# Kernel tuning notes

Hardware: AMD Instinct MI355X
Metric: run time of the kernel (lower is better)

The kernel has to match this reference:

```python
import jax, jax.numpy as jnp
import numpy as np

B, T, F, H = 16, 512, 32, 128
EPS = 1e-5


def _layer_norm(y, g, b):
    mu = jnp.mean(y, axis=-1, keepdims=True)
    var = jnp.mean(jnp.square(y - mu), axis=-1, keepdims=True)
    return (y - mu) * jax.lax.rsqrt(var + EPS) * g + b


def setup_inputs() -> dict:
    key = jax.random.key(0)
    ks = jax.random.split(key, 16)
    s = 0.1  # small param scale
    return {
        "x": jax.random.normal(ks[0], (B, T, F), jnp.float32),
        # weight GRN (input_size == hidden == F, skip is Identity)
        "wg_fc1_w": jax.random.normal(ks[1], (F, F), jnp.float32) * s,
        "wg_fc1_b": jnp.zeros((F,), jnp.float32),
        "wg_fc2_w": jax.random.normal(ks[2], (2 * F, F), jnp.float32) * s,
        "wg_fc2_b": jnp.zeros((2 * F,), jnp.float32),
        "wg_ln_g": jnp.ones((F,), jnp.float32),
        "wg_ln_b": jnp.zeros((F,), jnp.float32),
        # per-feature GRNs (input_size=1 -> hidden H), batched over F
        "f_fc1_w": jax.random.normal(ks[3], (F, H), jnp.float32) * s,   # torch Linear(1,H).weight squeezed
        "f_fc1_b": jax.random.normal(ks[4], (F, H), jnp.float32) * s,
        "f_fc2_w": jax.random.normal(ks[5], (F, 2 * H, H), jnp.float32) * s,
        "f_fc2_b": jax.random.normal(ks[6], (F, 2 * H), jnp.float32) * s,
        "f_skip_w": jax.random.normal(ks[7], (F, H), jnp.float32) * s,  # Linear(1,H).weight squeezed
        "f_skip_b": jax.random.normal(ks[8], (F, H), jnp.float32) * s,
        "f_ln_g": jnp.ones((F, H), jnp.float32),
        "f_ln_b": jnp.zeros((F, H), jnp.float32),
    }


def reference(x, wg_fc1_w, wg_fc1_b, wg_fc2_w, wg_fc2_b, wg_ln_g, wg_ln_b,
              f_fc1_w, f_fc1_b, f_fc2_w, f_fc2_b, f_skip_w, f_skip_b,
              f_ln_g, f_ln_b):
    # --- weight GRN over the feature axis: [B,T,F] -> [B,T,F] ---
    h = jax.nn.elu(jnp.einsum('btf,gf->btg', x, wg_fc1_w) + wg_fc1_b)
    h2 = jnp.einsum('btg,kg->btk', h, wg_fc2_w) + wg_fc2_b  # [B,T,2F]
    a, g = jnp.split(h2, 2, axis=-1)
    glu = a * jax.nn.sigmoid(g)
    weights = jax.nn.softmax(_layer_norm(x + glu, wg_ln_g, wg_ln_b), axis=-1)  # [B,T,F]

    # --- all F per-feature GRNs batched (input width 1) ---
    xe = x[..., None]                                   # [B,T,F,1]
    h = jax.nn.elu(xe * f_fc1_w + f_fc1_b)              # [B,T,F,H]
    h2 = jnp.einsum('btfh,fgh->btfg', h, f_fc2_w) + f_fc2_b  # [B,T,F,2H]
    a, g = jnp.split(h2, 2, axis=-1)
    glu = a * jax.nn.sigmoid(g)                         # [B,T,F,H]
    res = xe * f_skip_w + f_skip_b                      # [B,T,F,H]
    y = _layer_norm(res + glu, f_ln_g, f_ln_b)          # per-feature LN params [F,H]

    # --- softmax-weighted combine ---
    return jnp.einsum('btf,btfh->bth', weights, y)      # [B,T,H]
```

## Files before the change

kernel.cpp:

```cpp
#include <hip/hip_runtime.h>
#include <cstdint>
#include <cstddef>

#define EPS 1e-5f

typedef float    f4    __attribute__((ext_vector_type(4)));
typedef _Float16 half8 __attribute__((ext_vector_type(8)));
typedef _Float16 half4 __attribute__((ext_vector_type(4)));

#define S_XS 33
#define LOG2E 1.44269504088896f

#define GLD_LDS16(gp, lp)                                        \
    __builtin_amdgcn_global_load_lds(                            \
        (const __attribute__((address_space(1))) void*)(gp),     \
        (__attribute__((address_space(3))) void*)(lp), 16, 0, 0)

__device__ __forceinline__ float fexp(float x)  { return __builtin_amdgcn_exp2f(x * LOG2E); }
__device__ __forceinline__ float frcp(float x)  { return __builtin_amdgcn_rcpf(x); }
__device__ __forceinline__ float frsq(float x)  { return __builtin_amdgcn_rsqf(x); }
__device__ __forceinline__ float fsig(float g)  { return frcp(1.f + __builtin_amdgcn_exp2f(g * -LOG2E)); }
__device__ __forceinline__ float felu(float t)  { return t > 0.f ? t : fexp(t) - 1.f; }

__global__ __launch_bounds__(256) void k_prep(
    const float* __restrict__ in_w2, _Float16* __restrict__ w2c,
    const float* __restrict__ x, const float* __restrict__ w1,
    const float* __restrict__ b1, const float* __restrict__ w2,
    const float* __restrict__ b2, const float* __restrict__ lng,
    const float* __restrict__ lnb,
    float* __restrict__ x_t, float* __restrict__ wts_t)
{
    __shared__ float w1s[32 * S_XS];
    __shared__ float w2s[64 * S_XS];
    __shared__ float xsW[32 * S_XS];
    __shared__ float ytile[32 * S_XS];

    const int bid = blockIdx.x;
    const int tid = threadIdx.x;

    if (bid < 512) {
        int t = bid * 256 + tid;
        int q  = t & 3;
        int g  = (t >> 2) & 255;
        int fk = t >> 10;
        int f = fk >> 2, kq = fk & 3;
        const float* ip = in_w2 + ((size_t)f * 256 + g) * 128 + kq * 32 + q * 8;
        f4 v0 = *(const f4*)ip, v1 = *(const f4*)(ip + 4);
        half8 h;
        #pragma unroll
        for (int i = 0; i < 4; ++i) { h[i] = (_Float16)v0[i]; h[4 + i] = (_Float16)v1[i]; }
        *(half8*)(w2c + (size_t)fk * 8192 + q * 2048 + g * 8) = h;
        return;
    }

    const int lane = tid & 63;
    const int f = lane & 31;
    const int wv = tid >> 6;
    const int row0 = (bid - 512) * 32;

    for (int i = tid; i < 1024; i += 256) {
        int r = i >> 5, c = i & 31;
        w1s[r * S_XS + c] = w1[i];
        xsW[r * S_XS + c] = x[(size_t)row0 * 32 + i];
    }
    for (int i = tid; i < 2048; i += 256) {
        int r = i >> 5, c = i & 31;
        w2s[r * S_XS + c] = w2[i];
    }
    const float b1f = b1[f], b2a = b2[f], b2g = b2[f + 32];
    const float lgf = lng[f], lbf = lnb[f];
    __syncthreads();

    for (int rr = 0; rr < 8; ++rr) {
        const int r = wv * 8 + rr;
        float acc = b1f;
        #pragma unroll
        for (int k = 0; k < 32; ++k)
            acc = fmaf(w1s[f * S_XS + k], xsW[r * S_XS + k], acc);
        float hval = felu(acc);

        float a = b2a, g = b2g;
        #pragma unroll
        for (int k = 0; k < 32; ++k) {
            float hk = __shfl(hval, k, 64);
            a = fmaf(w2s[f * S_XS + k], hk, a);
            g = fmaf(w2s[(f + 32) * S_XS + k], hk, g);
        }
        float xv = xsW[r * S_XS + f];
        float v = xv + a * fsig(g);

        float s = v;
        #pragma unroll
        for (int o = 1; o < 64; o <<= 1) s += __shfl_xor(s, o, 64);
        float mu = s * (1.f / 64.f);
        float d = v - mu;
        float sq = d * d;
        #pragma unroll
        for (int o = 1; o < 64; o <<= 1) sq += __shfl_xor(sq, o, 64);
        float y = d * frsq(sq * (1.f / 64.f) + EPS) * lgf + lbf;

        float m = y;
        #pragma unroll
        for (int o = 1; o < 64; o <<= 1) m = fmaxf(m, __shfl_xor(m, o, 64));
        float e = fexp(y - m);
        float se = e;
        #pragma unroll
        for (int o = 1; o < 64; o <<= 1) se += __shfl_xor(se, o, 64);
        if (lane < 32) ytile[r * S_XS + f] = e * 2.f * frcp(se);
    }
    __syncthreads();
    for (int i = tid; i < 1024; i += 256) {
        int ff = i >> 5, r = i & 31;
        x_t[(size_t)ff * 8192 + row0 + r]   = xsW[r * S_XS + ff];
        wts_t[(size_t)ff * 8192 + row0 + r] = ytile[r * S_XS + ff];
    }
}

__global__ __launch_bounds__(256, 3) void k_main(
    const _Float16* __restrict__ w2c,
    const float* __restrict__ x_t,
    const float* __restrict__ wts_t,
    const float* __restrict__ fc1w, const float* __restrict__ fc1b,
    const float* __restrict__ fc2b,
    const float* __restrict__ skw, const float* __restrict__ skb,
    const float* __restrict__ lng, const float* __restrict__ lnb,
    float* __restrict__ out)
{
    __shared__ __align__(16) _Float16 bchunk[2][8192];

    const int tid = threadIdx.x;
    const int fbase = (blockIdx.x >> 7) * 4;
    const int row0 = (blockIdx.x & 127) * 64;

    const int lane = tid & 63;
    const int wv = tid >> 6;
    const int l15 = lane & 15;
    const int q = lane >> 4;
    const int boff = q * 2048 + l15 * 8;

    auto stage = [&](int c) {
        const _Float16* gp = w2c + ((size_t)(fbase + (c >> 2)) * 4 + (c & 3)) * 8192;
        #pragma unroll
        for (int r = 0; r < 4; ++r)
            GLD_LDS16(gp + (r * 256 + tid) * 8,
                      &bchunk[c & 1][(r * 256 + tid) * 8]);
    };

    float out_acc[8][4];
    #pragma unroll
    for (int nt = 0; nt < 8; ++nt)
        #pragma unroll
        for (int rg = 0; rg < 4; ++rg) out_acc[nt][rg] = 0.f;

    stage(0);
    __syncthreads();

    int c = 0;
    for (int fi = 0; fi < 4; ++fi) {
        const int f = fbase + fi;
        const float* xcol = x_t + (size_t)f * 8192 + row0 + wv * 16;
        const float* wcol = wts_t + (size_t)f * 8192 + row0 + wv * 16;
        const float xvA = xcol[l15];

        half8 A[4];
        #pragma unroll
        for (int kq = 0; kq < 4; ++kq) {
            const float* wp = fc1w + f * 128 + kq * 32 + 8 * q;
            const float* bp = fc1b + f * 128 + kq * 32 + 8 * q;
            f4 w0 = *(const f4*)wp, w1v = *(const f4*)(wp + 4);
            f4 b0 = *(const f4*)bp, b1v = *(const f4*)(bp + 4);
            #pragma unroll
            for (int j = 0; j < 4; ++j) {
                A[kq][j]     = (_Float16)felu(fmaf(xvA, w0[j], b0[j]));
                A[kq][4 + j] = (_Float16)felu(fmaf(xvA, w1v[j], b1v[j]));
            }
        }

        f4 acc[16];
        #pragma unroll
        for (int nt = 0; nt < 8; ++nt) {
            const int h = nt * 16 + l15;
            float ba = fc2b[f * 256 + h];
            float bg = fc2b[f * 256 + 128 + h];
            #pragma unroll
            for (int rg = 0; rg < 4; ++rg) { acc[nt][rg] = ba; acc[nt + 8][rg] = bg; }
        }

        #pragma unroll
        for (int kq = 0; kq < 4; ++kq, ++c) {
            if (c + 1 < 16) stage(c + 1);
            const _Float16* bb = &bchunk[c & 1][boff];
            #pragma unroll
            for (int nt = 0; nt < 16; ++nt) {
                half8 B = *(const half8*)(bb + nt * 128);
                acc[nt] = __builtin_amdgcn_mfma_f32_16x16x32_f16(A[kq], B, acc[nt], 0, 0, 0);
            }
            __syncthreads();
        }

        f4 xr = *(const f4*)(xcol + 4 * q);
        f4 wr = *(const f4*)(wcol + 4 * q);
        float s[4] = {0.f, 0.f, 0.f, 0.f}, sq[4] = {0.f, 0.f, 0.f, 0.f};
        #pragma unroll
        for (int nt = 0; nt < 8; ++nt) {
            const int h = nt * 16 + l15;
            float sw = skw[f * 128 + h];
            float sb = skb[f * 128 + h];
            #pragma unroll
            for (int rg = 0; rg < 4; ++rg) {
                float a = acc[nt][rg];
                float g = acc[nt + 8][rg];
                float val = fmaf(xr[rg], sw, sb) + a * fsig(g);
                acc[nt][rg] = val;
                s[rg] += val;
                sq[rg] = fmaf(val, val, sq[rg]);
            }
        }
        #pragma unroll
        for (int o = 1; o < 16; o <<= 1) {
            #pragma unroll
            for (int rg = 0; rg < 4; ++rg) {
                s[rg] += __shfl_xor(s[rg], o, 64);
                sq[rg] += __shfl_xor(sq[rg], o, 64);
            }
        }
        float mu[4], c1[4];
        #pragma unroll
        for (int rg = 0; rg < 4; ++rg) {
            mu[rg] = s[rg] * (1.f / 128.f);
            float var = sq[rg] * (1.f / 128.f) - mu[rg] * mu[rg];
            c1[rg] = wr[rg] * frsq(fmaxf(var, 0.f) + EPS);
        }
        #pragma unroll
        for (int nt = 0; nt < 8; ++nt) {
            const int h = nt * 16 + l15;
            float lg = lng[f * 128 + h];
            float lb = lnb[f * 128 + h];
            #pragma unroll
            for (int rg = 0; rg < 4; ++rg) {
                float u = (acc[nt][rg] - mu[rg]) * c1[rg];
                out_acc[nt][rg] = fmaf(u, lg, fmaf(wr[rg], lb, out_acc[nt][rg]));
            }
        }
    }

    #pragma unroll
    for (int nt = 0; nt < 8; ++nt) {
        #pragma unroll
        for (int rg = 0; rg < 4; ++rg) {
            const int r = row0 + wv * 16 + 4 * q + rg;
            atomicAdd(&out[(size_t)r * 128 + nt * 16 + l15], out_acc[nt][rg]);
        }
    }
}

extern "C" void kernel_launch(void* const* d_in, const int* in_sizes, int n_in,
                              void* d_out, int out_size, void* d_ws, size_t ws_size,
                              hipStream_t stream) {
    const float* x     = (const float*)d_in[0];
    const float* wg1w  = (const float*)d_in[1];
    const float* wg1b  = (const float*)d_in[2];
    const float* wg2w  = (const float*)d_in[3];
    const float* wg2b  = (const float*)d_in[4];
    const float* wglng = (const float*)d_in[5];
    const float* wglnb = (const float*)d_in[6];
    const float* fc1w  = (const float*)d_in[7];
    const float* fc1b  = (const float*)d_in[8];
    const float* fc2w  = (const float*)d_in[9];
    const float* fc2b  = (const float*)d_in[10];
    const float* skw   = (const float*)d_in[11];
    const float* skb   = (const float*)d_in[12];
    const float* lng   = (const float*)d_in[13];
    const float* lnb   = (const float*)d_in[14];
    float* out = (float*)d_out;

    char* ws = (char*)d_ws;
    _Float16* w2c = (_Float16*)ws;
    float* x_t    = (float*)(ws + (2u << 20));
    float* wts_t  = (float*)(ws + (3u << 20));

    k_prep<<<dim3(768), dim3(256), 0, stream>>>(fc2w, w2c, x, wg1w, wg1b,
                                                wg2w, wg2b, wglng, wglnb,
                                                x_t, wts_t);
    hipMemsetAsync(out, 0, (size_t)out_size * sizeof(float), stream);
    k_main<<<dim3(1024), dim3(256), 0, stream>>>(w2c, x_t, wts_t, fc1w, fc1b,
                                                 fc2b, skw, skb, lng, lnb, out);
}
```

Baseline: 164.8 us.

## Double rows per k_main block and fold output zeroing into prep kernel

Each k_main wave now processes two 16-row M-tiles that share every staged fc2 weight chunk, halving the grid to 512 blocks. Each block therefore stages half as much weight data from global memory per row, and LDS B-fragment reads are amortized over two MFMAs. Launch bounds drop to 2 blocks per CU to allow the doubled accumulator registers. The separate hipMemsetAsync is replaced by 16 extra zeroing blocks in k_prep, removing one stream operation. The risks are lower occupancy and fewer blocks to fill the GPU.

```diff
diff --git a/kernel.cpp b/kernel.cpp
--- a/kernel.cpp
+++ b/kernel.cpp
@@ -28,7 +28,8 @@
     const float* __restrict__ b1, const float* __restrict__ w2,
     const float* __restrict__ b2, const float* __restrict__ lng,
     const float* __restrict__ lnb,
-    float* __restrict__ x_t, float* __restrict__ wts_t)
+    float* __restrict__ x_t, float* __restrict__ wts_t,
+    float* __restrict__ outp)
 {
     __shared__ float w1s[32 * S_XS];
     __shared__ float w2s[64 * S_XS];
@@ -53,6 +54,14 @@
         return;
     }
 
+    if (bid >= 768) {
+        int t = (bid - 768) * 256 + tid;
+        f4 z; z[0] = 0.f; z[1] = 0.f; z[2] = 0.f; z[3] = 0.f;
+        for (int i = t; i < 262144; i += 4096)
+            *(f4*)(outp + (size_t)i * 4) = z;
+        return;
+    }
+
     const int lane = tid & 63;
     const int f = lane & 31;
     const int wv = tid >> 6;
@@ -116,7 +125,7 @@
     }
 }
 
-__global__ __launch_bounds__(256, 3) void k_main(
+__global__ __launch_bounds__(256, 2) void k_main(
     const _Float16* __restrict__ w2c,
     const float* __restrict__ x_t,
     const float* __restrict__ wts_t,
@@ -129,8 +138,8 @@
     __shared__ __align__(16) _Float16 bchunk[2][8192];
 
     const int tid = threadIdx.x;
-    const int fbase = (blockIdx.x >> 7) * 4;
-    const int row0 = (blockIdx.x & 127) * 64;
+    const int fbase = (blockIdx.x >> 6) * 4;
+    const int row0 = (blockIdx.x & 63) * 128;
 
     const int lane = tid & 63;
     const int wv = tid >> 6;
@@ -146,11 +155,13 @@
                       &bchunk[c & 1][(r * 256 + tid) * 8]);
     };
 
-    float out_acc[8][4];
+    float out_acc[2][8][4];
     #pragma unroll
-    for (int nt = 0; nt < 8; ++nt)
-        #pragma unroll
-        for (int rg = 0; rg < 4; ++rg) out_acc[nt][rg] = 0.f;
+    for (int ss = 0; ss < 2; ++ss)
+        #pragma unroll
+        for (int nt = 0; nt < 8; ++nt)
+            #pragma unroll
+            for (int rg = 0; rg < 4; ++rg) out_acc[ss][nt][rg] = 0.f;
 
     stage(0);
     __syncthreads();
@@ -158,11 +169,12 @@
     int c = 0;
     for (int fi = 0; fi < 4; ++fi) {
         const int f = fbase + fi;
-        const float* xcol = x_t + (size_t)f * 8192 + row0 + wv * 16;
-        const float* wcol = wts_t + (size_t)f * 8192 + row0 + wv * 16;
-        const float xvA = xcol[l15];
-
-        half8 A[4];
+        const float* xcol = x_t + (size_t)f * 8192 + row0 + wv * 32;
+        const float* wcol = wts_t + (size_t)f * 8192 + row0 + wv * 32;
+        const float xvA0 = xcol[l15];
+        const float xvA1 = xcol[16 + l15];
+
+        half8 A0[4], A1[4];
         #pragma unroll
         for (int kq = 0; kq < 4; ++kq) {
             const float* wp = fc1w + f * 128 + kq * 32 + 8 * q;
@@ -171,19 +183,28 @@
             f4 b0 = *(const f4*)bp, b1v = *(const f4*)(bp + 4);
             #pragma unroll
             for (int j = 0; j < 4; ++j) {
-                A[kq][j]     = (_Float16)felu(fmaf(xvA, w0[j], b0[j]));
-                A[kq][4 + j] = (_Float16)felu(fmaf(xvA, w1v[j], b1v[j]));
-            }
-        }
-
-        f4 acc[16];
+                float t0 = fmaf(xvA0, w0[j], b0[j]);
+                float t1 = fmaf(xvA0, w1v[j], b1v[j]);
+                A0[kq][j]     = (_Float16)felu(t0);
+                A0[kq][4 + j] = (_Float16)felu(t1);
+                float u0 = fmaf(xvA1, w0[j], b0[j]);
+                float u1 = fmaf(xvA1, w1v[j], b1v[j]);
+                A1[kq][j]     = (_Float16)felu(u0);
+                A1[kq][4 + j] = (_Float16)felu(u1);
+            }
+        }
+
+        f4 acc[2][16];
         #pragma unroll
         for (int nt = 0; nt < 8; ++nt) {
             const int h = nt * 16 + l15;
             float ba = fc2b[f * 256 + h];
             float bg = fc2b[f * 256 + 128 + h];
             #pragma unroll
-            for (int rg = 0; rg < 4; ++rg) { acc[nt][rg] = ba; acc[nt + 8][rg] = bg; }
+            for (int rg = 0; rg < 4; ++rg) {
+                acc[0][nt][rg] = ba; acc[0][nt + 8][rg] = bg;
+                acc[1][nt][rg] = ba; acc[1][nt + 8][rg] = bg;
+            }
         }
 
         #pragma unroll
@@ -193,63 +214,81 @@
             #pragma unroll
             for (int nt = 0; nt < 16; ++nt) {
                 half8 B = *(const half8*)(bb + nt * 128);
-                acc[nt] = __builtin_amdgcn_mfma_f32_16x16x32_f16(A[kq], B, acc[nt], 0, 0, 0);
+                acc[0][nt] = __builtin_amdgcn_mfma_f32_16x16x32_f16(A0[kq], B, acc[0][nt], 0, 0, 0);
+                acc[1][nt] = __builtin_amdgcn_mfma_f32_16x16x32_f16(A1[kq], B, acc[1][nt], 0, 0, 0);
             }
             __syncthreads();
         }
 
-        f4 xr = *(const f4*)(xcol + 4 * q);
-        f4 wr = *(const f4*)(wcol + 4 * q);
-        float s[4] = {0.f, 0.f, 0.f, 0.f}, sq[4] = {0.f, 0.f, 0.f, 0.f};
+        f4 xr[2], wr[2];
+        xr[0] = *(const f4*)(xcol + 4 * q);
+        xr[1] = *(const f4*)(xcol + 16 + 4 * q);
+        wr[0] = *(const f4*)(wcol + 4 * q);
+        wr[1] = *(const f4*)(wcol + 16 + 4 * q);
+        float s[2][4] = {{0.f,0.f,0.f,0.f},{0.f,0.f,0.f,0.f}};
+        float sq[2][4] = {{0.f,0.f,0.f,0.f},{0.f,0.f,0.f,0.f}};
         #pragma unroll
         for (int nt = 0; nt < 8; ++nt) {
             const int h = nt * 16 + l15;
             float sw = skw[f * 128 + h];
             float sb = skb[f * 128 + h];
             #pragma unroll
+            for (int ss = 0; ss < 2; ++ss) {
+                #pragma unroll
+                for (int rg = 0; rg < 4; ++rg) {
+                    float a = acc[ss][nt][rg];
+                    float g = acc[ss][nt + 8][rg];
+                    float val = fmaf(xr[ss][rg], sw, sb) + a * fsig(g);
+                    acc[ss][nt][rg] = val;
+                    s[ss][rg] += val;
+                    sq[ss][rg] = fmaf(val, val, sq[ss][rg]);
+                }
+            }
+        }
+        #pragma unroll
+        for (int o = 1; o < 16; o <<= 1) {
+            #pragma unroll
+            for (int ss = 0; ss < 2; ++ss)
+                #pragma unroll
+                for (int rg = 0; rg < 4; ++rg) {
+                    s[ss][rg] += __shfl_xor(s[ss][rg], o, 64);
+                    sq[ss][rg] += __shfl_xor(sq[ss][rg], o, 64);
+                }
+        }
+        float mu[2][4], c1[2][4];
+        #pragma unroll
+        for (int ss = 0; ss < 2; ++ss)
+            #pragma unroll
             for (int rg = 0; rg < 4; ++rg) {
-                float a = acc[nt][rg];
-                float g = acc[nt + 8][rg];
-                float val = fmaf(xr[rg], sw, sb) + a * fsig(g);
-                acc[nt][rg] = val;
-                s[rg] += val;
-                sq[rg] = fmaf(val, val, sq[rg]);
-            }
-        }
-        #pragma unroll
-        for (int o = 1; o < 16; o <<= 1) {
-            #pragma unroll
-            for (int rg = 0; rg < 4; ++rg) {
-                s[rg] += __shfl_xor(s[rg], o, 64);
-                sq[rg] += __shfl_xor(sq[rg], o, 64);
-            }
-        }
-        float mu[4], c1[4];
-        #pragma unroll
-        for (int rg = 0; rg < 4; ++rg) {
-            mu[rg] = s[rg] * (1.f / 128.f);
-            float var = sq[rg] * (1.f / 128.f) - mu[rg] * mu[rg];
-            c1[rg] = wr[rg] * frsq(fmaxf(var, 0.f) + EPS);
-        }
+                mu[ss][rg] = s[ss][rg] * (1.f / 128.f);
+                float var = sq[ss][rg] * (1.f / 128.f) - mu[ss][rg] * mu[ss][rg];
+                c1[ss][rg] = wr[ss][rg] * frsq(fmaxf(var, 0.f) + EPS);
+            }
         #pragma unroll
         for (int nt = 0; nt < 8; ++nt) {
             const int h = nt * 16 + l15;
             float lg = lng[f * 128 + h];
             float lb = lnb[f * 128 + h];
             #pragma unroll
+            for (int ss = 0; ss < 2; ++ss)
+                #pragma unroll
+                for (int rg = 0; rg < 4; ++rg) {
+                    float u = (acc[ss][nt][rg] - mu[ss][rg]) * c1[ss][rg];
+                    out_acc[ss][nt][rg] = fmaf(u, lg,
+                        fmaf(wr[ss][rg], lb, out_acc[ss][nt][rg]));
+                }
+        }
+    }
+
+    #pragma unroll
+    for (int ss = 0; ss < 2; ++ss) {
+        #pragma unroll
+        for (int nt = 0; nt < 8; ++nt) {
+            #pragma unroll
             for (int rg = 0; rg < 4; ++rg) {
-                float u = (acc[nt][rg] - mu[rg]) * c1[rg];
-                out_acc[nt][rg] = fmaf(u, lg, fmaf(wr[rg], lb, out_acc[nt][rg]));
-            }
-        }
-    }
-
-    #pragma unroll
-    for (int nt = 0; nt < 8; ++nt) {
-        #pragma unroll
-        for (int rg = 0; rg < 4; ++rg) {
-            const int r = row0 + wv * 16 + 4 * q + rg;
-            atomicAdd(&out[(size_t)r * 128 + nt * 16 + l15], out_acc[nt][rg]);
+                const int r = row0 + wv * 32 + ss * 16 + 4 * q + rg;
+                atomicAdd(&out[(size_t)r * 128 + nt * 16 + l15], out_acc[ss][nt][rg]);
+            }
         }
     }
 }
@@ -279,10 +318,9 @@
     float* x_t    = (float*)(ws + (2u << 20));
     float* wts_t  = (float*)(ws + (3u << 20));
 
-    k_prep<<<dim3(768), dim3(256), 0, stream>>>(fc2w, w2c, x, wg1w, wg1b,
+    k_prep<<<dim3(784), dim3(256), 0, stream>>>(fc2w, w2c, x, wg1w, wg1b,
                                                 wg2w, wg2b, wglng, wglnb,
-                                                x_t, wts_t);
-    hipMemsetAsync(out, 0, (size_t)out_size * sizeof(float), stream);
-    k_main<<<dim3(1024), dim3(256), 0, stream>>>(w2c, x_t, wts_t, fc1w, fc1b,
-                                                 fc2b, skw, skb, lng, lnb, out);
+                                                x_t, wts_t, out);
+    k_main<<<dim3(512), dim3(256), 0, stream>>>(w2c, x_t, wts_t, fc1w, fc1b,
+                                                fc2b, skw, skb, lng, lnb, out);
 }
```

After: 168.8 us. 1.02x slower.

## Stage two K-chunks per barrier and fold output zeroing into prep kernel

Applied to the files above, without the earlier changes.

The fc2 weight staging in k_main now loads two K-chunks (32 KB) per phase into a double buffer of 64 KB LDS, which halves the number of __syncthreads barriers per feature. The separate hipMemsetAsync of the output is removed, and extra blocks in k_prep zero the output buffer instead, saving one launch. The doubled LDS footprint may cut how many blocks fit per CU below the launch_bounds target of 3.

```diff
diff --git a/kernel.cpp b/kernel.cpp
--- a/kernel.cpp
+++ b/kernel.cpp
@@ -28,7 +28,8 @@
     const float* __restrict__ b1, const float* __restrict__ w2,
     const float* __restrict__ b2, const float* __restrict__ lng,
     const float* __restrict__ lnb,
-    float* __restrict__ x_t, float* __restrict__ wts_t)
+    float* __restrict__ x_t, float* __restrict__ wts_t,
+    float* __restrict__ outp)
 {
     __shared__ float w1s[32 * S_XS];
     __shared__ float w2s[64 * S_XS];
@@ -50,6 +51,14 @@
         #pragma unroll
         for (int i = 0; i < 4; ++i) { h[i] = (_Float16)v0[i]; h[4 + i] = (_Float16)v1[i]; }
         *(half8*)(w2c + (size_t)fk * 8192 + q * 2048 + g * 8) = h;
+        return;
+    }
+
+    if (bid >= 768) {
+        int t = (bid - 768) * 256 + tid;
+        f4 z; z[0] = 0.f; z[1] = 0.f; z[2] = 0.f; z[3] = 0.f;
+        for (int i = t; i < 262144; i += 4096)
+            *(f4*)(outp + (size_t)i * 4) = z;
         return;
     }
 
@@ -126,7 +135,7 @@
     const float* __restrict__ lng, const float* __restrict__ lnb,
     float* __restrict__ out)
 {
-    __shared__ __align__(16) _Float16 bchunk[2][8192];
+    __shared__ __align__(16) _Float16 bbuf[2][16384];
 
     const int tid = threadIdx.x;
     const int fbase = (blockIdx.x >> 7) * 4;
@@ -138,12 +147,12 @@
     const int q = lane >> 4;
     const int boff = q * 2048 + l15 * 8;
 
-    auto stage = [&](int c) {
-        const _Float16* gp = w2c + ((size_t)(fbase + (c >> 2)) * 4 + (c & 3)) * 8192;
-        #pragma unroll
-        for (int r = 0; r < 4; ++r)
-            GLD_LDS16(gp + (r * 256 + tid) * 8,
-                      &bchunk[c & 1][(r * 256 + tid) * 8]);
+    auto stage = [&](int ph) {
+        const _Float16* gp = w2c + ((size_t)(fbase + (ph >> 1)) * 4 + (ph & 1) * 2) * 8192;
+        _Float16* lp = bbuf[ph & 1];
+        #pragma unroll
+        for (int r = 0; r < 8; ++r)
+            GLD_LDS16(gp + (r * 256 + tid) * 8, lp + (r * 256 + tid) * 8);
     };
 
     float out_acc[8][4];
@@ -155,7 +164,6 @@
     stage(0);
     __syncthreads();
 
-    int c = 0;
     for (int fi = 0; fi < 4; ++fi) {
         const int f = fbase + fi;
         const float* xcol = x_t + (size_t)f * 8192 + row0 + wv * 16;
@@ -187,13 +195,18 @@
         }
 
         #pragma unroll
-        for (int kq = 0; kq < 4; ++kq, ++c) {
-            if (c + 1 < 16) stage(c + 1);
-            const _Float16* bb = &bchunk[c & 1][boff];
-            #pragma unroll
-            for (int nt = 0; nt < 16; ++nt) {
-                half8 B = *(const half8*)(bb + nt * 128);
-                acc[nt] = __builtin_amdgcn_mfma_f32_16x16x32_f16(A[kq], B, acc[nt], 0, 0, 0);
+        for (int half = 0; half < 2; ++half) {
+            const int ph = fi * 2 + half;
+            if (ph + 1 < 8) stage(ph + 1);
+            #pragma unroll
+            for (int kqL = 0; kqL < 2; ++kqL) {
+                const int kq = half * 2 + kqL;
+                const _Float16* bb = &bbuf[ph & 1][kqL * 8192 + boff];
+                #pragma unroll
+                for (int nt = 0; nt < 16; ++nt) {
+                    half8 B = *(const half8*)(bb + nt * 128);
+                    acc[nt] = __builtin_amdgcn_mfma_f32_16x16x32_f16(A[kq], B, acc[nt], 0, 0, 0);
+                }
             }
             __syncthreads();
         }
@@ -279,10 +292,9 @@
     float* x_t    = (float*)(ws + (2u << 20));
     float* wts_t  = (float*)(ws + (3u << 20));
 
-    k_prep<<<dim3(768), dim3(256), 0, stream>>>(fc2w, w2c, x, wg1w, wg1b,
+    k_prep<<<dim3(784), dim3(256), 0, stream>>>(fc2w, w2c, x, wg1w, wg1b,
                                                 wg2w, wg2b, wglng, wglnb,
-                                                x_t, wts_t);
-    hipMemsetAsync(out, 0, (size_t)out_size * sizeof(float), stream);
+                                                x_t, wts_t, out);
     k_main<<<dim3(1024), dim3(256), 0, stream>>>(w2c, x_t, wts_t, fc1w, fc1b,
                                                  fc2b, skw, skb, lng, lnb, out);
 }
```

Result: slower. 187.5 us (+13.8%).
